# Performance work log

Hardware: AMD Instinct MI355X
Metric: run time of the kernel (lower is better)

## Reference

```python
import jax, jax.numpy as jnp
import numpy as np

D_MODEL = 512
D_FFN = 1024
B, N = 8, 2048


def setup_inputs() -> dict:
    key = jax.random.key(0)
    k1, k2, k3, k4, k5, k6 = jax.random.split(key, 6)
    x = jax.random.normal(k1, (B, N, D_MODEL), dtype=jnp.float32)
    interaction_mask = jax.random.randint(k2, (B, N, N), 0, 2).astype(jnp.float32)
    s1 = 1.0 / np.sqrt(D_MODEL)
    s2 = 1.0 / np.sqrt(D_FFN)
    W1 = jax.random.uniform(k3, (D_MODEL, D_FFN), jnp.float32, -s1, s1)
    b1 = jax.random.uniform(k4, (D_FFN,), jnp.float32, -s1, s1)
    W2 = jax.random.uniform(k5, (D_FFN, 3 * D_MODEL), jnp.float32, -s2, s2)
    b2 = jax.random.uniform(k6, (3 * D_MODEL,), jnp.float32, -s2, s2)
    return {"x": x, "interaction_mask": interaction_mask,
            "W1": W1, "b1": b1, "W2": W2, "b2": b2}


def reference(x, interaction_mask, W1, b1, W2, b2):
    # 2-layer FFN: Linear -> ReLU -> Linear (identity)
    h = jax.nn.relu(x @ W1 + b1)           # [B, N, d_ffn]
    kqv = h @ W2 + b2                        # [B, N, 3*d_model]
    k, q, v = jnp.split(kqv, 3, axis=-1)     # each [B, N, d_model]
    scale = D_MODEL ** -0.5
    # softmax-free scaled dot-product
    attn = jnp.einsum("bqd,bkd->bqk", q, k) * scale  # [B, N, N]
    attn = attn * interaction_mask
    return jnp.einsum("bqk,bkd->bqd", attn, v)        # [B, N, d_model]
```

## Files before the change

kernel.cpp:

```cpp
#include <hip/hip_runtime.h>
#include <hip/hip_bf16.h>

typedef __attribute__((ext_vector_type(8))) short bf16x8;
typedef __attribute__((ext_vector_type(4))) float f32x4;

#define NB 8
#define NN 2048
#define DM 512
#define DF 1024

__device__ __forceinline__ ushort f2b(float f) {
  union { __hip_bfloat16 h; ushort u; } c;
  c.h = __float2bfloat16(f);
  return c.u;
}
__device__ __forceinline__ float b2f(ushort u) {
  union { ushort u; __hip_bfloat16 h; } c;
  c.u = u;
  return __bfloat162float(c.h);
}

typedef __attribute__((address_space(1))) const void gvoid_t;
typedef __attribute__((address_space(3))) void svoid_t;
__device__ __forceinline__ void gload16(const void* g, void* s) {
  __builtin_amdgcn_global_load_lds((gvoid_t*)g, (svoid_t*)s, 16, 0, 0);
}

__device__ __forceinline__ void gemm_core_128(
    const ushort* __restrict__ A, const ushort* __restrict__ B,
    int K, int brow, int bcol, f32x4 (&acc)[4][4], ushort* smem)
{
  ushort* As = smem;
  ushort* Bs = smem + 128 * 64;
  const int tid = threadIdx.x;
  const int w = tid >> 6;
  const int l = tid & 63;
  const int sr = (w << 3) + (l >> 3);
  const int sc = (((l & 7) ^ (l >> 3)) << 3);
  char* AsB = (char*)As;
  char* BsB = (char*)Bs;
  const int fr = l & 15;
  const int arow = ((w >> 1) << 6) + fr;
  const int brw  = ((w & 1) << 6) + fr;

#pragma unroll
  for (int m = 0; m < 4; m++)
#pragma unroll
    for (int n = 0; n < 4; n++)
      acc[m][n] = (f32x4){0.f, 0.f, 0.f, 0.f};

  const ushort* Ap = A + (long)(brow + sr) * K + sc;
  const ushort* Bp = B + (long)(bcol + sr) * K + sc;
  const int nkt = K >> 6;
  for (int kt = 0; kt < nkt; ++kt) {
#pragma unroll
    for (int i = 0; i < 4; i++) {
      gload16(Ap + (long)i * 32 * K, AsB + i * 4096 + (w << 10));
      gload16(Bp + (long)i * 32 * K, BsB + i * 4096 + (w << 10));
    }
    Ap += 64; Bp += 64;
    __syncthreads();
#pragma unroll
    for (int kk = 0; kk < 2; kk++) {
      const int cx = ((((kk << 2) + (l >> 4)) ^ (l & 7)) << 4);
      bf16x8 a[4], b[4];
#pragma unroll
      for (int m = 0; m < 4; m++)
        a[m] = *(const bf16x8*)(AsB + (arow + m * 16) * 128 + cx);
#pragma unroll
      for (int n = 0; n < 4; n++)
        b[n] = *(const bf16x8*)(BsB + (brw + n * 16) * 128 + cx);
#pragma unroll
      for (int m = 0; m < 4; m++)
#pragma unroll
        for (int n = 0; n < 4; n++)
          acc[m][n] = __builtin_amdgcn_mfma_f32_16x16x32_bf16(a[m], b[n], acc[m][n], 0, 0, 0);
    }
    __syncthreads();
  }
}

__device__ __forceinline__ void acc_to_lds_bf16(f32x4 (&acc)[4][4], ushort* smem) {
  const int tid = threadIdx.x, w = tid >> 6, l = tid & 63;
  const int r0l = ((w >> 1) << 6) + ((l >> 4) << 2);
  const int c0l = ((w & 1) << 6) + (l & 15);
#pragma unroll
  for (int n = 0; n < 4; n++)
#pragma unroll
    for (int m = 0; m < 4; m++)
#pragma unroll
      for (int j = 0; j < 4; j++)
        smem[(r0l + m * 16 + j) * 128 + (c0l + n * 16)] = f2b(acc[m][n][j]);
}


__global__ __launch_bounds__(256) void k_cvt(const float* __restrict__ in,
                                             ushort* __restrict__ out) {
  const long i = ((long)blockIdx.x * 256 + threadIdx.x) << 2;
  const float4 v = *(const float4*)(in + i);
  ushort4 o;
  o.x = f2b(v.x); o.y = f2b(v.y); o.z = f2b(v.z); o.w = f2b(v.w);
  *(ushort4*)(out + i) = o;
}

__device__ __forceinline__ float ld2f(const float* p, long i) { return p[i]; }
__device__ __forceinline__ float ld2f(const __hip_bfloat16* p, long i) { return __bfloat162float(p[i]); }

template <typename TIN>
__global__ __launch_bounds__(256) void k_tr(const TIN* __restrict__ in, ushort* __restrict__ out,
                                            int R, int C, long inB, long outB) {
  __shared__ float t[32][33];
  const long b = blockIdx.z;
  const TIN* ip = in + b * inB;
  ushort* op = out + b * outB;
  const int c0 = blockIdx.x << 5, r0 = blockIdx.y << 5;
  const int tx = threadIdx.x & 31, ty = threadIdx.x >> 5;
#pragma unroll
  for (int j = 0; j < 32; j += 8)
    t[ty + j][tx] = ld2f(ip, (long)(r0 + ty + j) * C + (c0 + tx));
  __syncthreads();
#pragma unroll
  for (int j = 0; j < 32; j += 8)
    op[(long)(c0 + ty + j) * R + (r0 + tx)] = f2b(t[tx][ty + j]);
}

__global__ __launch_bounds__(256) void k_gemm1(const ushort* __restrict__ xb,
                                               const ushort* __restrict__ w1t,
                                               const float* __restrict__ b1,
                                               ushort* __restrict__ hb) {
  __shared__ ushort smem[128 * 128];
  f32x4 acc[4][4];
  const int brow = blockIdx.x << 7, bcol = blockIdx.y << 7;
  gemm_core_128(xb, w1t, DM, brow, bcol, acc, smem);
  const int tid = threadIdx.x, w = tid >> 6, l = tid & 63;
  const int c0l = ((w & 1) << 6) + (l & 15);
#pragma unroll
  for (int n = 0; n < 4; n++) {
    const float bias = b1[bcol + c0l + n * 16];
#pragma unroll
    for (int m = 0; m < 4; m++)
#pragma unroll
      for (int j = 0; j < 4; j++) {
        float v = acc[m][n][j] + bias;
        acc[m][n][j] = v > 0.f ? v : 0.f;
      }
  }
  acc_to_lds_bf16(acc, smem);
  __syncthreads();
  const int rb = tid >> 4, cb = tid & 15;
#pragma unroll
  for (int i = 0; i < 8; i++) {
    const int row = i * 16 + rb;
    bf16x8 s = *(const bf16x8*)(smem + row * 128 + cb * 8);
    *(bf16x8*)(hb + (long)(brow + row) * DF + bcol + cb * 8) = s;
  }
}

__global__ __launch_bounds__(256) void k_gemm2(const ushort* __restrict__ hb,
                                               const ushort* __restrict__ w2t,
                                               const float* __restrict__ b2,
                                               ushort* __restrict__ kb,
                                               ushort* __restrict__ qb,
                                               ushort* __restrict__ vb) {
  __shared__ ushort smem[128 * 128];
  f32x4 acc[4][4];
  const int brow = blockIdx.x << 7, bcol = blockIdx.y << 7;
  gemm_core_128(hb, w2t, DF, brow, bcol, acc, smem);
  const int seg = bcol >> 9;
  ushort* dst = (seg == 0) ? kb : ((seg == 1) ? qb : vb);
  const float sc = (seg == 1) ? 0.04419417382415922f : 1.0f;
  const int tid = threadIdx.x, w = tid >> 6, l = tid & 63;
  const int c0l = ((w & 1) << 6) + (l & 15);
#pragma unroll
  for (int n = 0; n < 4; n++) {
    const float bias = b2[bcol + c0l + n * 16];
#pragma unroll
    for (int m = 0; m < 4; m++)
#pragma unroll
      for (int j = 0; j < 4; j++)
        acc[m][n][j] = (acc[m][n][j] + bias) * sc;
  }
  acc_to_lds_bf16(acc, smem);
  __syncthreads();
  const int rb = tid >> 4, cb = tid & 15;
  const int clb = bcol - (seg << 9);
#pragma unroll
  for (int i = 0; i < 8; i++) {
    const int row = i * 16 + rb;
    bf16x8 s = *(const bf16x8*)(smem + row * 128 + cb * 8);
    *(bf16x8*)(dst + (long)(brow + row) * DM + clb + cb * 8) = s;
  }
}

__global__ __launch_bounds__(256) void k_qk(const ushort* __restrict__ qb,
                                            const ushort* __restrict__ kb,
                                            const float* __restrict__ mask,
                                            ushort* __restrict__ Sbuf) {
  __shared__ ushort smem[128 * 128];
  const int batch = blockIdx.z;
  const ushort* A = qb + (long)batch * NN * DM;
  const ushort* Bm = kb + (long)batch * NN * DM;
  const float* mk = mask + (long)batch * NN * NN;
  ushort* S = Sbuf + (long)batch * NN * NN;
  f32x4 acc[4][4];
  const int brow = blockIdx.x << 7, bcol = blockIdx.y << 7;
  gemm_core_128(A, Bm, DM, brow, bcol, acc, smem);
  acc_to_lds_bf16(acc, smem);
  __syncthreads();
  const int tid = threadIdx.x, rb = tid >> 4, cb = tid & 15;
#pragma unroll
  for (int i = 0; i < 8; i++) {
    const int row = i * 16 + rb;
    const long goff = (long)(brow + row) * NN + bcol + cb * 8;
    bf16x8 s = *(const bf16x8*)(smem + row * 128 + cb * 8);
    const float4 m0 = *(const float4*)(mk + goff);
    const float4 m1 = *(const float4*)(mk + goff + 4);
    bf16x8 o;
    o[0] = (short)f2b(b2f((ushort)s[0]) * m0.x);
    o[1] = (short)f2b(b2f((ushort)s[1]) * m0.y);
    o[2] = (short)f2b(b2f((ushort)s[2]) * m0.z);
    o[3] = (short)f2b(b2f((ushort)s[3]) * m0.w);
    o[4] = (short)f2b(b2f((ushort)s[4]) * m1.x);
    o[5] = (short)f2b(b2f((ushort)s[5]) * m1.y);
    o[6] = (short)f2b(b2f((ushort)s[6]) * m1.z);
    o[7] = (short)f2b(b2f((ushort)s[7]) * m1.w);
    *(bf16x8*)(S + goff) = o;
  }
}

__global__ __launch_bounds__(256) void k_pv(const ushort* __restrict__ Sbuf,
                                            const ushort* __restrict__ vtb,
                                            float* __restrict__ out) {
  __shared__ ushort smem[128 * 128];
  const int batch = blockIdx.z;
  const ushort* A = Sbuf + (long)batch * NN * NN;
  const ushort* Bm = vtb + (long)batch * DM * NN;
  float* op = out + (long)batch * NN * DM;
  f32x4 acc[4][4];
  const int brow = blockIdx.x << 7, bcol = blockIdx.y << 7;
  gemm_core_128(A, Bm, NN, brow, bcol, acc, smem);
  const int tid = threadIdx.x, w = tid >> 6, l = tid & 63;
  const int r0 = brow + ((w >> 1) << 6) + ((l >> 4) << 2);
  const int c0 = bcol + ((w & 1) << 6) + (l & 15);
#pragma unroll
  for (int n = 0; n < 4; n++) {
    const int c = c0 + n * 16;
#pragma unroll
    for (int m = 0; m < 4; m++) {
      const int r = r0 + m * 16;
#pragma unroll
      for (int j = 0; j < 4; j++)
        op[(long)(r + j) * DM + c] = acc[m][n][j];
    }
  }
}

extern "C" void kernel_launch(void* const* d_in, const int* in_sizes, int n_in,
                              void* d_out, int out_size, void* d_ws, size_t ws_size,
                              hipStream_t stream) {
  const float* x    = (const float*)d_in[0];
  const float* mask = (const float*)d_in[1];
  const float* W1   = (const float*)d_in[2];
  const float* b1   = (const float*)d_in[3];
  const float* W2   = (const float*)d_in[4];
  const float* b2   = (const float*)d_in[5];
  float* out = (float*)d_out;

  char* ws = (char*)d_ws;
  size_t off = 0;
  auto alloc = [&](size_t n) { char* p = ws + off; off += (n + 255) & ~(size_t)255; return p; };
  ushort* xb  = (ushort*)alloc((size_t)NB * NN * DM * 2);
  ushort* hb  = (ushort*)alloc((size_t)NB * NN * DF * 2);
  ushort* w1t = (ushort*)alloc((size_t)DF * DM * 2);
  ushort* w2t = (ushort*)alloc((size_t)3 * DM * DF * 2);
  ushort* kb  = (ushort*)alloc((size_t)NB * NN * DM * 2);
  ushort* qb  = (ushort*)alloc((size_t)NB * NN * DM * 2);
  ushort* vb  = (ushort*)alloc((size_t)NB * NN * DM * 2);
  ushort* vtb = (ushort*)alloc((size_t)NB * NN * DM * 2);
  ushort* Sbuf = (ushort*)alloc((size_t)NB * NN * NN * 2);

  k_cvt<<<dim3(8192), dim3(256), 0, stream>>>(x, xb);
  k_tr<float><<<dim3(DF / 32, DM / 32, 1), dim3(256), 0, stream>>>(W1, w1t, DM, DF, 0, 0);
  k_tr<float><<<dim3(3 * DM / 32, DF / 32, 1), dim3(256), 0, stream>>>(W2, w2t, DF, 3 * DM, 0, 0);
  k_gemm1<<<dim3(NB * NN / 128, DF / 128), dim3(256), 0, stream>>>(xb, w1t, b1, hb);
  k_gemm2<<<dim3(NB * NN / 128, 3 * DM / 128), dim3(256), 0, stream>>>(hb, w2t, b2, kb, qb, vb);
  k_tr<__hip_bfloat16><<<dim3(DM / 32, NN / 32, NB), dim3(256), 0, stream>>>(
      (const __hip_bfloat16*)vb, vtb, NN, DM, (long)NN * DM, (long)DM * NN);
  k_qk<<<dim3(NN / 128, NN / 128, NB), dim3(256), 0, stream>>>(qb, kb, mask, Sbuf);
  k_pv<<<dim3(NN / 128, DM / 128, NB), dim3(256), 0, stream>>>(Sbuf, vtb, out);
}
```

Baseline: 222.9 us.

## Fuse QK^T masking and PV into a single flash-style attention kernel

Replaces the separate QK and PV kernels with one fused kernel. Each 512-thread block keeps a 64-row Q tile in LDS, loops over 128-wide KV tiles, computes masked scores into an LDS P tile, then multiplies by V^T into register accumulators. This removes the write and re-read of the 8x2048x2048 bf16 score buffer and one launch. In exchange the grid drops to only 256 blocks with heavy LDS use (144KB), there are many syncthreads per tile with no load/compute overlap, and K/V are re-read from global by each Q block.

```diff
diff --git a/kernel.cpp b/kernel.cpp
--- a/kernel.cpp
+++ b/kernel.cpp
@@ -192,67 +192,136 @@
   }
 }
 
-__global__ __launch_bounds__(256) void k_qk(const ushort* __restrict__ qb,
-                                            const ushort* __restrict__ kb,
-                                            const float* __restrict__ mask,
-                                            ushort* __restrict__ Sbuf) {
-  __shared__ ushort smem[128 * 128];
-  const int batch = blockIdx.z;
-  const ushort* A = qb + (long)batch * NN * DM;
-  const ushort* Bm = kb + (long)batch * NN * DM;
-  const float* mk = mask + (long)batch * NN * NN;
-  ushort* S = Sbuf + (long)batch * NN * NN;
-  f32x4 acc[4][4];
-  const int brow = blockIdx.x << 7, bcol = blockIdx.y << 7;
-  gemm_core_128(A, Bm, DM, brow, bcol, acc, smem);
-  acc_to_lds_bf16(acc, smem);
-  __syncthreads();
-  const int tid = threadIdx.x, rb = tid >> 4, cb = tid & 15;
-#pragma unroll
-  for (int i = 0; i < 8; i++) {
-    const int row = i * 16 + rb;
-    const long goff = (long)(brow + row) * NN + bcol + cb * 8;
-    bf16x8 s = *(const bf16x8*)(smem + row * 128 + cb * 8);
-    const float4 m0 = *(const float4*)(mk + goff);
-    const float4 m1 = *(const float4*)(mk + goff + 4);
-    bf16x8 o;
-    o[0] = (short)f2b(b2f((ushort)s[0]) * m0.x);
-    o[1] = (short)f2b(b2f((ushort)s[1]) * m0.y);
-    o[2] = (short)f2b(b2f((ushort)s[2]) * m0.z);
-    o[3] = (short)f2b(b2f((ushort)s[3]) * m0.w);
-    o[4] = (short)f2b(b2f((ushort)s[4]) * m1.x);
-    o[5] = (short)f2b(b2f((ushort)s[5]) * m1.y);
-    o[6] = (short)f2b(b2f((ushort)s[6]) * m1.z);
-    o[7] = (short)f2b(b2f((ushort)s[7]) * m1.w);
-    *(bf16x8*)(S + goff) = o;
-  }
-}
-
-__global__ __launch_bounds__(256) void k_pv(const ushort* __restrict__ Sbuf,
-                                            const ushort* __restrict__ vtb,
-                                            float* __restrict__ out) {
-  __shared__ ushort smem[128 * 128];
-  const int batch = blockIdx.z;
-  const ushort* A = Sbuf + (long)batch * NN * NN;
-  const ushort* Bm = vtb + (long)batch * DM * NN;
+__global__ __launch_bounds__(512, 2) void k_attn(const ushort* __restrict__ qb,
+                                                 const ushort* __restrict__ kb,
+                                                 const ushort* __restrict__ vtb,
+                                                 const float* __restrict__ mask,
+                                                 float* __restrict__ out) {
+  __shared__ ushort smem[73728];
+  char* QsB = (char*)smem;
+  char* KsB = (char*)smem + 65536;
+  char* VsB = (char*)smem + 65536 + 32768;
+  char* PsB = (char*)smem + 65536 + 65536;
+
+  const int tid = threadIdx.x, w = tid >> 6, l = tid & 63;
+  const int fr = l & 15;
+  const int batch = blockIdx.x & 7;
+  const int qrow0 = (blockIdx.x >> 3) << 6;
+  const ushort* qp = qb + (long)batch * NN * DM;
+  const ushort* kp = kb + (long)batch * NN * DM;
+  const ushort* vp = vtb + (long)batch * DM * NN;
+  const float* mp = mask + (long)batch * NN * NN;
   float* op = out + (long)batch * NN * DM;
-  f32x4 acc[4][4];
-  const int brow = blockIdx.x << 7, bcol = blockIdx.y << 7;
-  gemm_core_128(A, Bm, NN, brow, bcol, acc, smem);
-  const int tid = threadIdx.x, w = tid >> 6, l = tid & 63;
-  const int r0 = brow + ((w >> 1) << 6) + ((l >> 4) << 2);
-  const int c0 = bcol + ((w & 1) << 6) + (l & 15);
-#pragma unroll
-  for (int n = 0; n < 4; n++) {
-    const int c = c0 + n * 16;
-#pragma unroll
-    for (int m = 0; m < 4; m++) {
-      const int r = r0 + m * 16;
+
+  f32x4 acc[8][2];
+#pragma unroll
+  for (int dc = 0; dc < 8; dc++)
+#pragma unroll
+    for (int f = 0; f < 2; f++)
+      acc[dc][f] = (f32x4){0.f, 0.f, 0.f, 0.f};
+
+  {
+    const int r = (w << 3) + (l >> 3);
+    const int scol = ((l & 7) ^ (l >> 3)) << 3;
+#pragma unroll
+    for (int i = 0; i < 8; i++)
+      gload16(qp + (long)(qrow0 + r) * DM + i * 64 + scol, QsB + i * 8192 + (w << 10));
+  }
+
+  for (int t = 0; t < 16; ++t) {
+    const int kv0 = t << 7;
+    float mreg[4][4];
+#pragma unroll
+    for (int m = 0; m < 4; m++)
 #pragma unroll
       for (int j = 0; j < 4; j++)
-        op[(long)(r + j) * DM + c] = acc[m][n][j];
-    }
-  }
+        mreg[m][j] = mp[(long)(qrow0 + m * 16 + ((l >> 4) << 2) + j) * NN + kv0 + (w << 4) + fr];
+
+    f32x4 sacc[4];
+#pragma unroll
+    for (int m = 0; m < 4; m++) sacc[m] = (f32x4){0.f, 0.f, 0.f, 0.f};
+
+#pragma unroll
+    for (int dch = 0; dch < 4; ++dch) {
+      __syncthreads();
+#pragma unroll
+      for (int i = 0; i < 4; ++i) {
+        const int sub = i >> 1;
+        const int r = ((w << 1) + (i & 1)) * 8 + (l >> 3);
+        const int scol = ((l & 7) ^ (l >> 3)) << 3;
+        gload16(kp + (long)(kv0 + r) * DM + ((dch << 1) + sub) * 64 + scol,
+                KsB + sub * 16384 + (((w << 1) + (i & 1)) << 10));
+      }
+      __syncthreads();
+#pragma unroll
+      for (int sub = 0; sub < 2; ++sub) {
+        const int dc = (dch << 1) + sub;
+#pragma unroll
+        for (int kk = 0; kk < 2; ++kk) {
+          const int cx = (((kk << 2) + (l >> 4)) ^ (l & 7)) << 4;
+          bf16x8 bfr = *(const bf16x8*)(KsB + sub * 16384 + ((w << 4) + fr) * 128 + cx);
+#pragma unroll
+          for (int m = 0; m < 4; m++) {
+            bf16x8 a = *(const bf16x8*)(QsB + dc * 8192 + ((m << 4) + fr) * 128 + cx);
+            sacc[m] = __builtin_amdgcn_mfma_f32_16x16x32_bf16(a, bfr, sacc[m], 0, 0, 0);
+          }
+        }
+      }
+    }
+
+#pragma unroll
+    for (int m = 0; m < 4; m++)
+#pragma unroll
+      for (int j = 0; j < 4; j++) {
+        const int row = (m << 4) + ((l >> 4) << 2) + j;
+        const int ch = (((w << 1) + ((l >> 3) & 1)) ^ (row & 15));
+        *(ushort*)(PsB + row * 256 + (ch << 4) + ((l & 7) << 1)) = f2b(sacc[m][j] * mreg[m][j]);
+      }
+
+#pragma unroll
+    for (int dch = 0; dch < 4; ++dch) {
+      __syncthreads();
+#pragma unroll
+      for (int i = 0; i < 4; ++i) {
+        const int sub = i >> 1;
+        const int r = ((w << 1) + (i & 1)) * 4 + (l >> 4);
+        const int scol = ((l & 15) ^ (r & 15)) << 3;
+        gload16(vp + (long)(((dch << 1) + sub) * 64 + r) * NN + kv0 + scol,
+                VsB + sub * 16384 + (((w << 1) + (i & 1)) << 10));
+      }
+      __syncthreads();
+#pragma unroll
+      for (int sub = 0; sub < 2; ++sub) {
+        const int dc = (dch << 1) + sub;
+#pragma unroll
+        for (int f = 0; f < 2; ++f) {
+          const int m = ((w >> 2) << 1) + f;
+          f32x4 o = acc[dc][f];
+#pragma unroll
+          for (int ks = 0; ks < 4; ++ks) {
+            const int cxp = (((ks << 2) + (l >> 4)) ^ (l & 15)) << 4;
+            bf16x8 pa = *(const bf16x8*)(PsB + ((m << 4) + fr) * 256 + cxp);
+            bf16x8 vb_ = *(const bf16x8*)(VsB + sub * 16384 + (((w & 3) << 4) + fr) * 256 + cxp);
+            o = __builtin_amdgcn_mfma_f32_16x16x32_bf16(pa, vb_, o, 0, 0, 0);
+          }
+          acc[dc][f] = o;
+        }
+      }
+    }
+  }
+
+#pragma unroll
+  for (int dc = 0; dc < 8; dc++)
+#pragma unroll
+    for (int f = 0; f < 2; f++) {
+      const int m = ((w >> 2) << 1) + f;
+#pragma unroll
+      for (int j = 0; j < 4; j++) {
+        const int row = qrow0 + (m << 4) + ((l >> 4) << 2) + j;
+        const int col = (dc << 6) + ((w & 3) << 4) + fr;
+        op[(long)row * DM + col] = acc[dc][f][j];
+      }
+    }
 }
 
 extern "C" void kernel_launch(void* const* d_in, const int* in_sizes, int n_in,
@@ -277,7 +346,6 @@
   ushort* qb  = (ushort*)alloc((size_t)NB * NN * DM * 2);
   ushort* vb  = (ushort*)alloc((size_t)NB * NN * DM * 2);
   ushort* vtb = (ushort*)alloc((size_t)NB * NN * DM * 2);
-  ushort* Sbuf = (ushort*)alloc((size_t)NB * NN * NN * 2);
 
   k_cvt<<<dim3(8192), dim3(256), 0, stream>>>(x, xb);
   k_tr<float><<<dim3(DF / 32, DM / 32, 1), dim3(256), 0, stream>>>(W1, w1t, DM, DF, 0, 0);
@@ -286,6 +354,5 @@
   k_gemm2<<<dim3(NB * NN / 128, 3 * DM / 128), dim3(256), 0, stream>>>(hb, w2t, b2, kb, qb, vb);
   k_tr<__hip_bfloat16><<<dim3(DM / 32, NN / 32, NB), dim3(256), 0, stream>>>(
       (const __hip_bfloat16*)vb, vtb, NN, DM, (long)NN * DM, (long)DM * NN);
-  k_qk<<<dim3(NN / 128, NN / 128, NB), dim3(256), 0, stream>>>(qb, kb, mask, Sbuf);
-  k_pv<<<dim3(NN / 128, DM / 128, NB), dim3(256), 0, stream>>>(Sbuf, vtb, out);
-}
+  k_attn<<<dim3(256), dim3(512), 0, stream>>>(qb, kb, vtb, mask, out);
+}
```

Measured after the change: 260.2 us. +16.7%, slower.

## Double-buffer LDS in GEMM core, prefetch mask early, swizzle QK block order

Applied to the files above, without the earlier changes.

The shared GEMM core now ping-pongs between two LDS buffers, so the global->LDS loads for the next K tile are issued before computing the current one, overlapping memory with MFMA. LDS per block doubles to 64KB, which may reduce occupancy. The QK kernel loads its mask tile into registers before the GEMM to hide that read latency, at the cost of extra registers. It also uses a 1D grid with a swizzle that spreads consecutive blocks across batches/XCDs.

```diff
diff --git a/kernel.cpp b/kernel.cpp
--- a/kernel.cpp
+++ b/kernel.cpp
@@ -30,18 +30,16 @@
     const ushort* __restrict__ A, const ushort* __restrict__ B,
     int K, int brow, int bcol, f32x4 (&acc)[4][4], ushort* smem)
 {
-  ushort* As = smem;
-  ushort* Bs = smem + 128 * 64;
   const int tid = threadIdx.x;
-  const int w = tid >> 6;
-  const int l = tid & 63;
+  const int w = tid >> 6, l = tid & 63;
   const int sr = (w << 3) + (l >> 3);
   const int sc = (((l & 7) ^ (l >> 3)) << 3);
-  char* AsB = (char*)As;
-  char* BsB = (char*)Bs;
   const int fr = l & 15;
   const int arow = ((w >> 1) << 6) + fr;
   const int brw  = ((w & 1) << 6) + fr;
+  char* base = (char*)smem;
+  char* A0 = base;          char* B0 = base + 16384;
+  char* A1 = base + 32768;  char* B1 = base + 49152;
 
 #pragma unroll
   for (int m = 0; m < 4; m++)
@@ -52,30 +50,41 @@
   const ushort* Ap = A + (long)(brow + sr) * K + sc;
   const ushort* Bp = B + (long)(bcol + sr) * K + sc;
   const int nkt = K >> 6;
-  for (int kt = 0; kt < nkt; ++kt) {
+
+  auto stage = [&](char* Ad, char* Bd, int kt) {
 #pragma unroll
     for (int i = 0; i < 4; i++) {
-      gload16(Ap + (long)i * 32 * K, AsB + i * 4096 + (w << 10));
-      gload16(Bp + (long)i * 32 * K, BsB + i * 4096 + (w << 10));
+      gload16(Ap + (long)i * 32 * K + kt * 64, Ad + i * 4096 + (w << 10));
+      gload16(Bp + (long)i * 32 * K + kt * 64, Bd + i * 4096 + (w << 10));
     }
-    Ap += 64; Bp += 64;
-    __syncthreads();
+  };
+  auto compute = [&](const char* As_, const char* Bs_) {
 #pragma unroll
     for (int kk = 0; kk < 2; kk++) {
       const int cx = ((((kk << 2) + (l >> 4)) ^ (l & 7)) << 4);
       bf16x8 a[4], b[4];
 #pragma unroll
       for (int m = 0; m < 4; m++)
-        a[m] = *(const bf16x8*)(AsB + (arow + m * 16) * 128 + cx);
+        a[m] = *(const bf16x8*)(As_ + (arow + m * 16) * 128 + cx);
 #pragma unroll
       for (int n = 0; n < 4; n++)
-        b[n] = *(const bf16x8*)(BsB + (brw + n * 16) * 128 + cx);
+        b[n] = *(const bf16x8*)(Bs_ + (brw + n * 16) * 128 + cx);
 #pragma unroll
       for (int m = 0; m < 4; m++)
 #pragma unroll
         for (int n = 0; n < 4; n++)
           acc[m][n] = __builtin_amdgcn_mfma_f32_16x16x32_bf16(a[m], b[n], acc[m][n], 0, 0, 0);
     }
+  };
+
+  stage(A0, B0, 0);
+  __syncthreads();
+  for (int kt = 0; kt < nkt; kt += 2) {
+    stage(A1, B1, kt + 1);
+    compute(A0, B0);
+    __syncthreads();
+    if (kt + 2 < nkt) stage(A0, B0, kt + 2);
+    compute(A1, B1);
     __syncthreads();
   }
 }
@@ -128,7 +137,7 @@
                                                const ushort* __restrict__ w1t,
                                                const float* __restrict__ b1,
                                                ushort* __restrict__ hb) {
-  __shared__ ushort smem[128 * 128];
+  __shared__ ushort smem[128 * 256];
   f32x4 acc[4][4];
   const int brow = blockIdx.x << 7, bcol = blockIdx.y << 7;
   gemm_core_128(xb, w1t, DM, brow, bcol, acc, smem);
@@ -162,7 +171,7 @@
                                                ushort* __restrict__ kb,
                                                ushort* __restrict__ qb,
                                                ushort* __restrict__ vb) {
-  __shared__ ushort smem[128 * 128];
+  __shared__ ushort smem[128 * 256];
   f32x4 acc[4][4];
   const int brow = blockIdx.x << 7, bcol = blockIdx.y << 7;
   gemm_core_128(hb, w2t, DF, brow, bcol, acc, smem);
@@ -196,34 +205,43 @@
                                             const ushort* __restrict__ kb,
                                             const float* __restrict__ mask,
                                             ushort* __restrict__ Sbuf) {
-  __shared__ ushort smem[128 * 128];
-  const int batch = blockIdx.z;
+  __shared__ ushort smem[128 * 256];
+  const int orig = blockIdx.x;
+  const int swz = (orig & 7) * 256 + (orig >> 3);
+  const int bx = swz & 15, by = (swz >> 4) & 15, batch = swz >> 8;
+  const int brow = bx << 7, bcol = by << 7;
   const ushort* A = qb + (long)batch * NN * DM;
   const ushort* Bm = kb + (long)batch * NN * DM;
   const float* mk = mask + (long)batch * NN * NN;
   ushort* S = Sbuf + (long)batch * NN * NN;
+
+  const int tid = threadIdx.x, rb = tid >> 4, cb = tid & 15;
+  float4 mreg[8][2];
+#pragma unroll
+  for (int i = 0; i < 8; i++) {
+    const long goff = (long)(brow + i * 16 + rb) * NN + bcol + cb * 8;
+    mreg[i][0] = *(const float4*)(mk + goff);
+    mreg[i][1] = *(const float4*)(mk + goff + 4);
+  }
+
   f32x4 acc[4][4];
-  const int brow = blockIdx.x << 7, bcol = blockIdx.y << 7;
   gemm_core_128(A, Bm, DM, brow, bcol, acc, smem);
   acc_to_lds_bf16(acc, smem);
   __syncthreads();
-  const int tid = threadIdx.x, rb = tid >> 4, cb = tid & 15;
 #pragma unroll
   for (int i = 0; i < 8; i++) {
     const int row = i * 16 + rb;
     const long goff = (long)(brow + row) * NN + bcol + cb * 8;
     bf16x8 s = *(const bf16x8*)(smem + row * 128 + cb * 8);
-    const float4 m0 = *(const float4*)(mk + goff);
-    const float4 m1 = *(const float4*)(mk + goff + 4);
     bf16x8 o;
-    o[0] = (short)f2b(b2f((ushort)s[0]) * m0.x);
-    o[1] = (short)f2b(b2f((ushort)s[1]) * m0.y);
-    o[2] = (short)f2b(b2f((ushort)s[2]) * m0.z);
-    o[3] = (short)f2b(b2f((ushort)s[3]) * m0.w);
-    o[4] = (short)f2b(b2f((ushort)s[4]) * m1.x);
-    o[5] = (short)f2b(b2f((ushort)s[5]) * m1.y);
-    o[6] = (short)f2b(b2f((ushort)s[6]) * m1.z);
-    o[7] = (short)f2b(b2f((ushort)s[7]) * m1.w);
+    o[0] = (short)f2b(b2f((ushort)s[0]) * mreg[i][0].x);
+    o[1] = (short)f2b(b2f((ushort)s[1]) * mreg[i][0].y);
+    o[2] = (short)f2b(b2f((ushort)s[2]) * mreg[i][0].z);
+    o[3] = (short)f2b(b2f((ushort)s[3]) * mreg[i][0].w);
+    o[4] = (short)f2b(b2f((ushort)s[4]) * mreg[i][1].x);
+    o[5] = (short)f2b(b2f((ushort)s[5]) * mreg[i][1].y);
+    o[6] = (short)f2b(b2f((ushort)s[6]) * mreg[i][1].z);
+    o[7] = (short)f2b(b2f((ushort)s[7]) * mreg[i][1].w);
     *(bf16x8*)(S + goff) = o;
   }
 }
@@ -231,7 +249,7 @@
 __global__ __launch_bounds__(256) void k_pv(const ushort* __restrict__ Sbuf,
                                             const ushort* __restrict__ vtb,
                                             float* __restrict__ out) {
-  __shared__ ushort smem[128 * 128];
+  __shared__ ushort smem[128 * 256];
   const int batch = blockIdx.z;
   const ushort* A = Sbuf + (long)batch * NN * NN;
   const ushort* Bm = vtb + (long)batch * DM * NN;
@@ -286,6 +304,6 @@
   k_gemm2<<<dim3(NB * NN / 128, 3 * DM / 128), dim3(256), 0, stream>>>(hb, w2t, b2, kb, qb, vb);
   k_tr<__hip_bfloat16><<<dim3(DM / 32, NN / 32, NB), dim3(256), 0, stream>>>(
       (const __hip_bfloat16*)vb, vtb, NN, DM, (long)NN * DM, (long)DM * NN);
-  k_qk<<<dim3(NN / 128, NN / 128, NB), dim3(256), 0, stream>>>(qb, kb, mask, Sbuf);
+  k_qk<<<dim3(2048), dim3(256), 0, stream>>>(qb, kb, mask, Sbuf);
   k_pv<<<dim3(NN / 128, DM / 128, NB), dim3(256), 0, stream>>>(Sbuf, vtb, out);
 }
```

After: 221.1 us. No clear change (-0.8%).
